# Kernel tuning notes

Measured on AMD Instinct MI355X. Metric: run time of the kernel, lower is better.

Reference implementation:

```python
import jax, jax.numpy as jnp
import numpy as np

EMBD_DIM = 1024
HEAD_SIZE = 64


def setup_inputs() -> dict:
    key = jax.random.key(0)
    kx, kq, kk, kv = jax.random.split(key, 4)
    x = jax.random.normal(kx, (4, 4096, EMBD_DIM), dtype=jnp.float32)
    # nn.Linear(embd_dim, head_size, bias=False) weights, stored as [C, H] so x @ W
    s = 1.0 / np.sqrt(EMBD_DIM)
    Wq = jax.random.uniform(kq, (EMBD_DIM, HEAD_SIZE), jnp.float32, -s, s)
    Wk = jax.random.uniform(kk, (EMBD_DIM, HEAD_SIZE), jnp.float32, -s, s)
    Wv = jax.random.uniform(kv, (EMBD_DIM, HEAD_SIZE), jnp.float32, -s, s)
    return {"x": x, "Wq": Wq, "Wk": Wk, "Wv": Wv}


def reference(x, Wq, Wk, Wv):
    # q,k,v: [B, T, H]
    q = jnp.einsum("btc,ch->bth", x, Wq)
    k = jnp.einsum("btc,ch->bth", x, Wk)
    v = jnp.einsum("btc,ch->bth", x, Wv)
    scale = k.shape[-1] ** -0.5
    # full [B, T, T] score matrix, as in the original naive implementation
    scores = jnp.einsum("bth,bsh->bts", q, k) * scale
    attn = jax.nn.softmax(scores, axis=-1)
    # dropout p=0.0 -> identity
    out = jnp.einsum("bts,bsh->bth", attn, v)  # [B, T, H]
    return out
```

## Files before the change

### kernel.cpp

```cpp
#include <hip/hip_runtime.h>
#include <hip/hip_bf16.h>

#define B_ 4
#define T_ 4096
#define C_ 1024
#define H_ 64

typedef float  f32x4  __attribute__((ext_vector_type(4)));
typedef short  bf16x8 __attribute__((ext_vector_type(8)));
typedef uint   u32x4  __attribute__((ext_vector_type(4)));

static __device__ __forceinline__ ushort f2bf(float f) {
  union { float f; uint u; } v; v.f = f;
  uint u = v.u;
  u += 0x7FFFu + ((u >> 16) & 1u);
  return (ushort)(u >> 16);
}

static __device__ __forceinline__ uint cvtpk(float s0, float s1) {
  uint r;
  asm("v_cvt_pk_bf16_f32 %0, %1, %2" : "=v"(r) : "v"(s0), "v"(s1));
  return r;
}

static __device__ __forceinline__ void gload_lds16(const void* g, void* l) {
  __builtin_amdgcn_global_load_lds(
      (const __attribute__((address_space(1))) unsigned int*)g,
      (__attribute__((address_space(3))) unsigned int*)l, 16, 0, 0);
}

#define MFMA(a, b, c) __builtin_amdgcn_mfma_f32_16x16x32_bf16(a, b, c, 0, 0, 0)
#define SBAR0() __builtin_amdgcn_sched_barrier(0)

__global__ __launch_bounds__(256) void wt_prep(const float* __restrict__ Wq,
                                               const float* __restrict__ Wk,
                                               const float* __restrict__ Wv,
                                               ushort* __restrict__ WtF) {
  int idx = blockIdx.x * 256 + threadIdx.x;
  int w = idx >> 16, idx2 = idx & 65535;
  int c = idx2 >> 6, n = idx2 & 63;
  const float* W = (w == 0) ? Wq : (w == 1) ? Wk : Wv;
  float v = W[idx2];
  if (w == 0) v *= 0.18033688011112042f;
  int c64 = c >> 6, kc = (c >> 5) & 1, g = (c >> 3) & 3, j = c & 7;
  int nt = n >> 4, l15 = n & 15;
  size_t dst = ((size_t)((((w * 16 + c64) * 2 + kc) * 4 + nt) * 64 + g * 16 + l15)) * 8 + j;
  WtF[dst] = f2bf(v);
}

__global__ __launch_bounds__(128) void qkv_proj(const float* __restrict__ x,
                                                const ushort* __restrict__ WtF,
                                                ushort* __restrict__ Qg,
                                                char* __restrict__ KaF,
                                                char* __restrict__ VaF) {
  __shared__ __align__(16) ushort wl[2][12288];
  const int tid = threadIdx.x;
  const int lane = tid & 63, wid = tid >> 6;
  const int l15 = lane & 15, g = lane >> 4;
  const int b = blockIdx.x >> 7, rt = blockIdx.x & 127;
  const int wrow = rt * 32 + wid * 16;

  f32x4 acc[3][4];
  #pragma unroll
  for (int w = 0; w < 3; w++)
    #pragma unroll
    for (int nt = 0; nt < 4; nt++) acc[w][nt] = (f32x4)0.0f;

  const float* xr = x + ((size_t)b * T_ + wrow + l15) * C_ + g * 8;

  auto stagew = [&](int buf, int c64) {
    const char* srcb = (const char*)WtF + (size_t)c64 * 8192;
    char* dstb = (char*)wl[buf];
    #pragma unroll
    for (int p = 0; p < 6; p++)
      #pragma unroll
      for (int q = 0; q < 2; q++) {
        int sub = (wid * 2 + q) * 1024 + lane * 16;
        gload_lds16(srcb + (p >> 1) * 131072 + (p & 1) * 4096 + sub,
                    dstb + p * 4096 + sub);
      }
  };

  f32x4 xp[3][4];
  auto xload = [&](int slot, int t) {
    const float* src = xr + t * 64;
    xp[slot][0] = *(const f32x4*)src;
    xp[slot][1] = *(const f32x4*)(src + 4);
    xp[slot][2] = *(const f32x4*)(src + 32);
    xp[slot][3] = *(const f32x4*)(src + 36);
  };

  stagew(0, 0);
  xload(0, 0);
  xload(1, 1);
  asm volatile("s_waitcnt vmcnt(8)" ::: "memory");
  __builtin_amdgcn_s_barrier();
  SBAR0();

  #pragma unroll
  for (int t = 0; t < 16; t++) {
    const int cur = t & 1;
    if (t < 15) stagew(cur ^ 1, t + 1);
    if (t < 14) xload((t + 2) % 3, t + 2);

    const int slot = t % 3;
    bf16x8 xa[2];
    #pragma unroll
    for (int kc = 0; kc < 2; kc++) {
      union { uint u[4]; bf16x8 v; } h;
      f32x4 c0 = xp[slot][2 * kc], c1 = xp[slot][2 * kc + 1];
      h.u[0] = cvtpk(c0[0], c0[1]); h.u[1] = cvtpk(c0[2], c0[3]);
      h.u[2] = cvtpk(c1[0], c1[1]); h.u[3] = cvtpk(c1[2], c1[3]);
      xa[kc] = h.v;
    }
    const char* wb = (const char*)wl[cur] + lane * 16;
    __builtin_amdgcn_s_setprio(1);
    #pragma unroll
    for (int w = 0; w < 3; w++)
      #pragma unroll
      for (int kc = 0; kc < 2; kc++)
        #pragma unroll
        for (int nt = 0; nt < 4; nt++) {
          bf16x8 wf = *(const bf16x8*)(wb + w * 8192 + kc * 4096 + nt * 1024);
          acc[w][nt] = MFMA(xa[kc], wf, acc[w][nt]);
        }
    __builtin_amdgcn_s_setprio(0);

    if (t < 15) {
      if (t < 14) asm volatile("s_waitcnt vmcnt(4)" ::: "memory");
      else        asm volatile("s_waitcnt vmcnt(0)" ::: "memory");
      __builtin_amdgcn_s_barrier();
      SBAR0();
    }
  }

  char* kdst = KaF + ((size_t)b * 64 + (rt >> 1)) * 8192;
  char* vdst = VaF + ((size_t)b * 128 + rt) * 4096;
  #pragma unroll
  for (int nt = 0; nt < 4; nt++) {
    int n = nt * 16 + l15;
    int kc = n >> 5, gp2 = (n >> 3) & 3, j2 = n & 7;
    #pragma unroll
    for (int r = 0; r < 4; r++) {
      int tt = wrow + g * 4 + r;
      Qg[((size_t)b * T_ + tt) * H_ + n] = f2bf(acc[0][nt][r]);
      int key = tt & 63;
      *(ushort*)(kdst + kc * 4096 + (key >> 4) * 1024 +
                 (gp2 * 16 + (key & 15)) * 16 + j2 * 2) = f2bf(acc[1][nt][r]);
      int k5 = tt & 31;
      int gp = ((k5 >> 4) << 1) | ((k5 >> 2) & 1);
      int js = ((k5 >> 3) & 1) * 4 + (k5 & 3);
      *(ushort*)(vdst + nt * 1024 + (gp * 16 + l15) * 16 + js * 2) = f2bf(acc[2][nt][r]);
    }
  }
}

__global__ __launch_bounds__(256) void attn(const ushort* __restrict__ Qg,
                                            const char* __restrict__ KaF,
                                            const char* __restrict__ VaF,
                                            ushort* __restrict__ Op,
                                            float* __restrict__ Ds,
                                            float* __restrict__ out,
                                            int KT) {
  __shared__ __align__(16) char kv[3][16384];
  const int tid = threadIdx.x;
  const int lane = tid & 63, wid = tid >> 6;
  const int bid = blockIdx.x;
  const int b = bid & 3;
  const int qt = (bid >> 2) & 31, s = bid >> 7;
  const int l15 = lane & 15, g = lane >> 4;

  bf16x8 qa[2][2];
  #pragma unroll
  for (int qs = 0; qs < 2; qs++) {
    const ushort* qp = Qg + ((size_t)b * T_ + qt * 128 + wid * 32 + qs * 16 + l15) * H_ + g * 8;
    qa[qs][0] = *(const bf16x8*)qp;
    qa[qs][1] = *(const bf16x8*)(qp + 32);
  }

  union { ushort u[8]; bf16x8 v; } ones_u;
  #pragma unroll
  for (int i = 0; i < 8; i++) ones_u.u[i] = 0x3F80;
  const bf16x8 ones = ones_u.v;

  f32x4 oacc[2][4];
  f32x4 dacc[2];
  #pragma unroll
  for (int qs = 0; qs < 2; qs++) {
    #pragma unroll
    for (int nt = 0; nt < 4; nt++) oacc[qs][nt] = (f32x4)0.0f;
    dacc[qs] = (f32x4)0.0f;
  }

  const char* kbase = KaF + (size_t)b * 64 * 8192;
  const char* vbase = VaF + (size_t)b * 128 * 4096;
  const int it0 = s * KT;

  auto stage = [&](int buf, int it) {
    char* dst = kv[buf] + tid * 16;
    const char* ks = kbase + (size_t)it * 8192 + tid * 16;
    const char* vs = vbase + (size_t)it * 8192 + tid * 16;
    gload_lds16(ks, dst);
    gload_lds16(ks + 4096, dst + 4096);
    gload_lds16(vs, dst + 8192);
    gload_lds16(vs + 4096, dst + 12288);
  };

  stage(0, it0);
  stage(1, it0 + 1);
  asm volatile("s_waitcnt vmcnt(4)" ::: "memory");
  __builtin_amdgcn_s_barrier();
  SBAR0();

  int cur = 0;
  for (int it = 0; it < KT; it++) {
    int pfb = cur + 2; if (pfb >= 3) pfb -= 3;
    if (it + 2 < KT) stage(pfb, it0 + it + 2);
    const char* kl = kv[cur];
    const char* vl = kv[cur] + 8192;

    f32x4 sacc[2][4];
    #pragma unroll
    for (int qs = 0; qs < 2; qs++)
      #pragma unroll
      for (int nt = 0; nt < 4; nt++) sacc[qs][nt] = (f32x4)0.0f;
    __builtin_amdgcn_s_setprio(1);
    #pragma unroll
    for (int nt = 0; nt < 4; nt++)
      #pragma unroll
      for (int kc = 0; kc < 2; kc++) {
        bf16x8 ka = *(const bf16x8*)(kl + kc * 4096 + nt * 1024 + lane * 16);
        sacc[0][nt] = MFMA(ka, qa[0][kc], sacc[0][nt]);
        sacc[1][nt] = MFMA(ka, qa[1][kc], sacc[1][nt]);
      }
    __builtin_amdgcn_s_setprio(0);

    #pragma unroll
    for (int kk = 0; kk < 2; kk++) {
      bf16x8 pf2[2];
      #pragma unroll
      for (int qs = 0; qs < 2; qs++) {
        f32x4 sa = sacc[qs][2 * kk], sb = sacc[qs][2 * kk + 1];
        uint x0 = cvtpk(__builtin_amdgcn_exp2f(sa[0]), __builtin_amdgcn_exp2f(sa[1]));
        uint x1 = cvtpk(__builtin_amdgcn_exp2f(sa[2]), __builtin_amdgcn_exp2f(sa[3]));
        uint y0 = cvtpk(__builtin_amdgcn_exp2f(sb[0]), __builtin_amdgcn_exp2f(sb[1]));
        uint y1 = cvtpk(__builtin_amdgcn_exp2f(sb[2]), __builtin_amdgcn_exp2f(sb[3]));
        asm volatile("v_permlane32_swap_b32 %0, %1" : "+v"(x0), "+v"(y0));
        asm volatile("v_permlane32_swap_b32 %0, %1" : "+v"(x1), "+v"(y1));
        union { uint u[4]; bf16x8 v; } pfu;
        pfu.u[0] = x0; pfu.u[1] = x1; pfu.u[2] = y0; pfu.u[3] = y1;
        pf2[qs] = pfu.v;
      }
      __builtin_amdgcn_s_setprio(1);
      #pragma unroll
      for (int ntd = 0; ntd < 4; ntd++) {
        bf16x8 va = *(const bf16x8*)(vl + kk * 4096 + ntd * 1024 + lane * 16);
        oacc[0][ntd] = MFMA(va, pf2[0], oacc[0][ntd]);
        oacc[1][ntd] = MFMA(va, pf2[1], oacc[1][ntd]);
      }
      dacc[0] = MFMA(ones, pf2[0], dacc[0]);
      dacc[1] = MFMA(ones, pf2[1], dacc[1]);
      __builtin_amdgcn_s_setprio(0);
    }

    if (it + 1 < KT) {
      if (it + 2 < KT) asm volatile("s_waitcnt vmcnt(4)" ::: "memory");
      else             asm volatile("s_waitcnt vmcnt(0)" ::: "memory");
      __builtin_amdgcn_s_barrier();
      SBAR0();
    }
    cur = cur + 1; if (cur >= 3) cur -= 3;
  }

  #pragma unroll
  for (int qs = 0; qs < 2; qs++) {
    float d = dacc[qs][0];
    const int q = qt * 128 + wid * 32 + qs * 16 + l15;
    if (Op != nullptr) {
      ushort* ob = Op + ((size_t)(s * 4 + b) * T_ + q) * H_;
      #pragma unroll
      for (int nt = 0; nt < 4; nt++) {
        uint2 pk;
        pk.x = cvtpk(oacc[qs][nt][0], oacc[qs][nt][1]);
        pk.y = cvtpk(oacc[qs][nt][2], oacc[qs][nt][3]);
        *(uint2*)(ob + nt * 16 + g * 4) = pk;
      }
      if (g == 0) Ds[(size_t)(s * 4 + b) * T_ + q] = d;
    } else {
      float inv = 1.0f / d;
      float* ob = out + ((size_t)b * T_ + q) * H_;
      #pragma unroll
      for (int nt = 0; nt < 4; nt++)
        #pragma unroll
        for (int r = 0; r < 4; r++) ob[nt * 16 + g * 4 + r] = oacc[qs][nt][r] * inv;
    }
  }
}

__global__ __launch_bounds__(256) void reduce_seg(const ushort* __restrict__ Op,
                                                  const float* __restrict__ Ds,
                                                  float* __restrict__ out, int seg) {
  int i = blockIdx.x * 256 + threadIdx.x;
  size_t e = (size_t)i * 4;
  int row = (int)(e >> 6);
  f32x4 o = (f32x4)0.0f;
  float d = 0.0f;
  for (int s = 0; s < seg; s++) {
    uint2 pk = *(const uint2*)(Op + (size_t)s * ((size_t)B_ * T_ * H_) + e);
    union { uint u; float f; } c0, c1, c2, c3;
    c0.u = (pk.x & 0xFFFFu) << 16; c1.u = (pk.x >> 16) << 16;
    c2.u = (pk.y & 0xFFFFu) << 16; c3.u = (pk.y >> 16) << 16;
    o[0] += c0.f; o[1] += c1.f; o[2] += c2.f; o[3] += c3.f;
    d += Ds[(size_t)s * ((size_t)B_ * T_) + row];
  }
  *(f32x4*)(out + e) = o * (1.0f / d);
}

extern "C" void kernel_launch(void* const* d_in, const int* in_sizes, int n_in,
                              void* d_out, int out_size, void* d_ws, size_t ws_size,
                              hipStream_t stream) {
  const float* x  = (const float*)d_in[0];
  const float* Wq = (const float*)d_in[1];
  const float* Wk = (const float*)d_in[2];
  const float* Wv = (const float*)d_in[3];
  float* out = (float*)d_out;

  char* ws = (char*)d_ws;
  size_t off = 0;
  auto take = [&](size_t n) -> void* {
    void* p = ws + off;
    off = (off + n + 255) & ~(size_t)255;
    return p;
  };
  ushort* Qg  = (ushort*)take((size_t)B_ * T_ * H_ * 2);
  char*   KaF = (char*)take((size_t)B_ * T_ * H_ * 2);
  char*   VaF = (char*)take((size_t)B_ * T_ * H_ * 2);
  ushort* WtF = (ushort*)take((size_t)3 * H_ * C_ * 2);

  int seg = 1;
  ushort* Op = nullptr;
  float* Ds = nullptr;
  for (int sg = 4; sg >= 2; sg >>= 1) {
    size_t need = off + (size_t)sg * B_ * T_ * H_ * 2 + 256 + (size_t)sg * B_ * T_ * 4 + 256;
    if (need <= ws_size) {
      seg = sg;
      Op = (ushort*)take((size_t)sg * B_ * T_ * H_ * 2);
      Ds = (float*)take((size_t)sg * B_ * T_ * 4);
      break;
    }
  }
  int KT = 64 / seg;

  wt_prep<<<768, 256, 0, stream>>>(Wq, Wk, Wv, WtF);
  qkv_proj<<<B_ * 128, 128, 0, stream>>>(x, WtF, Qg, KaF, VaF);
  attn<<<B_ * (T_ / 128) * seg, 256, 0, stream>>>(Qg, KaF, VaF, Op, Ds, out, KT);
  if (Op) reduce_seg<<<(B_ * T_ * H_ / 4 + 255) / 256, 256, 0, stream>>>(Op, Ds, out, seg);
}
```

Baseline: 55.29 us.

## Double rows per wave in QKV projection to reuse staged weights

Each wave in qkv_proj now computes two 16-row subtiles, so every weight fragment read from LDS feeds two MFMAs, and the grid is halved. The x prefetch moves from a three-slot, two-ahead scheme to a two-slot, one-ahead double buffer, with scheduling barriers around the loads and an adjusted vmcnt wait. The aim is to cut LDS weight traffic and per-block weight staging. In exchange there are fewer blocks (256 on a large GPU), higher register pressure from doubled accumulators, and shallower latency hiding for the x loads.

```diff
diff --git a/kernel.cpp b/kernel.cpp
--- a/kernel.cpp
+++ b/kernel.cpp
@@ -57,16 +57,19 @@
   const int tid = threadIdx.x;
   const int lane = tid & 63, wid = tid >> 6;
   const int l15 = lane & 15, g = lane >> 4;
-  const int b = blockIdx.x >> 7, rt = blockIdx.x & 127;
-  const int wrow = rt * 32 + wid * 16;
-
-  f32x4 acc[3][4];
-  #pragma unroll
-  for (int w = 0; w < 3; w++)
-    #pragma unroll
-    for (int nt = 0; nt < 4; nt++) acc[w][nt] = (f32x4)0.0f;
-
-  const float* xr = x + ((size_t)b * T_ + wrow + l15) * C_ + g * 8;
+  const int b = blockIdx.x >> 6, rt = blockIdx.x & 63;
+  const int wrow = rt * 64 + wid * 32;
+
+  f32x4 acc[2][3][4];
+  #pragma unroll
+  for (int su = 0; su < 2; su++)
+    #pragma unroll
+    for (int w = 0; w < 3; w++)
+      #pragma unroll
+      for (int nt = 0; nt < 4; nt++) acc[su][w][nt] = (f32x4)0.0f;
+
+  const float* xr0 = x + ((size_t)b * T_ + wrow + l15) * C_ + g * 8;
+  const float* xr1 = xr0 + (size_t)16 * C_;
 
   auto stagew = [&](int buf, int c64) {
     const char* srcb = (const char*)WtF + (size_t)c64 * 8192;
@@ -81,18 +84,24 @@
       }
   };
 
-  f32x4 xp[3][4];
+  f32x4 xp[2][2][4];
   auto xload = [&](int slot, int t) {
-    const float* src = xr + t * 64;
-    xp[slot][0] = *(const f32x4*)src;
-    xp[slot][1] = *(const f32x4*)(src + 4);
-    xp[slot][2] = *(const f32x4*)(src + 32);
-    xp[slot][3] = *(const f32x4*)(src + 36);
+    const float* s0 = xr0 + t * 64;
+    xp[slot][0][0] = *(const f32x4*)s0;
+    xp[slot][0][1] = *(const f32x4*)(s0 + 4);
+    xp[slot][0][2] = *(const f32x4*)(s0 + 32);
+    xp[slot][0][3] = *(const f32x4*)(s0 + 36);
+    const float* s1 = xr1 + t * 64;
+    xp[slot][1][0] = *(const f32x4*)s1;
+    xp[slot][1][1] = *(const f32x4*)(s1 + 4);
+    xp[slot][1][2] = *(const f32x4*)(s1 + 32);
+    xp[slot][1][3] = *(const f32x4*)(s1 + 36);
   };
 
   stagew(0, 0);
+  SBAR0();
   xload(0, 0);
-  xload(1, 1);
+  SBAR0();
   asm volatile("s_waitcnt vmcnt(8)" ::: "memory");
   __builtin_amdgcn_s_barrier();
   SBAR0();
@@ -100,19 +109,25 @@
   #pragma unroll
   for (int t = 0; t < 16; t++) {
     const int cur = t & 1;
-    if (t < 15) stagew(cur ^ 1, t + 1);
-    if (t < 14) xload((t + 2) % 3, t + 2);
-
-    const int slot = t % 3;
-    bf16x8 xa[2];
-    #pragma unroll
-    for (int kc = 0; kc < 2; kc++) {
-      union { uint u[4]; bf16x8 v; } h;
-      f32x4 c0 = xp[slot][2 * kc], c1 = xp[slot][2 * kc + 1];
-      h.u[0] = cvtpk(c0[0], c0[1]); h.u[1] = cvtpk(c0[2], c0[3]);
-      h.u[2] = cvtpk(c1[0], c1[1]); h.u[3] = cvtpk(c1[2], c1[3]);
-      xa[kc] = h.v;
-    }
+    if (t < 15) {
+      stagew(cur ^ 1, t + 1);
+      SBAR0();
+      xload(cur ^ 1, t + 1);
+      SBAR0();
+    }
+
+    bf16x8 xa[2][2];
+    #pragma unroll
+    for (int su = 0; su < 2; su++)
+      #pragma unroll
+      for (int kc = 0; kc < 2; kc++) {
+        union { uint u[4]; bf16x8 v; } h;
+        f32x4 c0 = xp[cur][su][2 * kc], c1 = xp[cur][su][2 * kc + 1];
+        h.u[0] = cvtpk(c0[0], c0[1]); h.u[1] = cvtpk(c0[2], c0[3]);
+        h.u[2] = cvtpk(c1[0], c1[1]); h.u[3] = cvtpk(c1[2], c1[3]);
+        xa[su][kc] = h.v;
+      }
+
     const char* wb = (const char*)wl[cur] + lane * 16;
     __builtin_amdgcn_s_setprio(1);
     #pragma unroll
@@ -122,35 +137,39 @@
         #pragma unroll
         for (int nt = 0; nt < 4; nt++) {
           bf16x8 wf = *(const bf16x8*)(wb + w * 8192 + kc * 4096 + nt * 1024);
-          acc[w][nt] = MFMA(xa[kc], wf, acc[w][nt]);
+          acc[0][w][nt] = MFMA(xa[0][kc], wf, acc[0][w][nt]);
+          acc[1][w][nt] = MFMA(xa[1][kc], wf, acc[1][w][nt]);
         }
     __builtin_amdgcn_s_setprio(0);
 
     if (t < 15) {
-      if (t < 14) asm volatile("s_waitcnt vmcnt(4)" ::: "memory");
-      else        asm volatile("s_waitcnt vmcnt(0)" ::: "memory");
+      SBAR0();
+      asm volatile("s_waitcnt vmcnt(8)" ::: "memory");
       __builtin_amdgcn_s_barrier();
       SBAR0();
     }
   }
 
-  char* kdst = KaF + ((size_t)b * 64 + (rt >> 1)) * 8192;
-  char* vdst = VaF + ((size_t)b * 128 + rt) * 4096;
-  #pragma unroll
-  for (int nt = 0; nt < 4; nt++) {
-    int n = nt * 16 + l15;
-    int kc = n >> 5, gp2 = (n >> 3) & 3, j2 = n & 7;
-    #pragma unroll
-    for (int r = 0; r < 4; r++) {
-      int tt = wrow + g * 4 + r;
-      Qg[((size_t)b * T_ + tt) * H_ + n] = f2bf(acc[0][nt][r]);
-      int key = tt & 63;
-      *(ushort*)(kdst + kc * 4096 + (key >> 4) * 1024 +
-                 (gp2 * 16 + (key & 15)) * 16 + j2 * 2) = f2bf(acc[1][nt][r]);
-      int k5 = tt & 31;
-      int gp = ((k5 >> 4) << 1) | ((k5 >> 2) & 1);
-      int js = ((k5 >> 3) & 1) * 4 + (k5 & 3);
-      *(ushort*)(vdst + nt * 1024 + (gp * 16 + l15) * 16 + js * 2) = f2bf(acc[2][nt][r]);
+  char* kdst = KaF + ((size_t)b * 64 + rt) * 8192;
+  char* vdst = VaF + ((size_t)b * 128 + rt * 2 + wid) * 4096;
+  #pragma unroll
+  for (int su = 0; su < 2; su++) {
+    #pragma unroll
+    for (int nt = 0; nt < 4; nt++) {
+      int n = nt * 16 + l15;
+      int kc = n >> 5, gp2 = (n >> 3) & 3, j2 = n & 7;
+      #pragma unroll
+      for (int r = 0; r < 4; r++) {
+        int tt = wrow + su * 16 + g * 4 + r;
+        Qg[((size_t)b * T_ + tt) * H_ + n] = f2bf(acc[su][0][nt][r]);
+        int key = tt & 63;
+        *(ushort*)(kdst + kc * 4096 + (key >> 4) * 1024 +
+                   (gp2 * 16 + (key & 15)) * 16 + j2 * 2) = f2bf(acc[su][1][nt][r]);
+        int k5 = tt & 31;
+        int gp = ((k5 >> 4) << 1) | ((k5 >> 2) & 1);
+        int js = ((k5 >> 3) & 1) * 4 + (k5 & 3);
+        *(ushort*)(vdst + nt * 1024 + (gp * 16 + l15) * 16 + js * 2) = f2bf(acc[su][2][nt][r]);
+      }
     }
   }
 }
@@ -352,7 +371,7 @@
   int KT = 64 / seg;
 
   wt_prep<<<768, 256, 0, stream>>>(Wq, Wk, Wv, WtF);
-  qkv_proj<<<B_ * 128, 128, 0, stream>>>(x, WtF, Qg, KaF, VaF);
+  qkv_proj<<<B_ * 64, 128, 0, stream>>>(x, WtF, Qg, KaF, VaF);
   attn<<<B_ * (T_ / 128) * seg, 256, 0, stream>>>(Qg, KaF, VaF, Op, Ds, out, KT);
   if (Op) reduce_seg<<<(B_ * T_ * H_ / 4 + 255) / 256, 256, 0, stream>>>(Op, Ds, out, seg);
 }
```

After: 58.62 us. 6.0% more time.
